# Performance work log

Measured on AMD Instinct MI355X. Metric: run time of the kernel, lower is better.

## Reference

```python
import jax, jax.numpy as jnp
import numpy as np

N_GRAPHS = 2048
BN_EPS = 1e-5


def _lin_init(k, fan_in, fan_out):
    kw, kb = jax.random.split(k)
    s = 1.0 / np.sqrt(fan_in)
    w = jax.random.uniform(kw, (fan_in, fan_out), minval=-s, maxval=s, dtype=jnp.float32)
    b = jax.random.uniform(kb, (fan_out,), minval=-s, maxval=s, dtype=jnp.float32)
    return w, b


def setup_inputs() -> dict:
    key = jax.random.key(0)
    ks = jax.random.split(key, 16)
    N, E, F, H, C = 100000, 600000, 7, 128, 2
    inp = {}
    inp["x"] = jax.random.normal(ks[0], (N, F), dtype=jnp.float32)
    inp["edge_index"] = jax.random.randint(ks[1], (2, E), 0, N)
    inp["edge_attr"] = jax.random.normal(ks[2], (E,), dtype=jnp.float32)  # ignored by GINConv
    inp["batch"] = jnp.sort(jax.random.randint(ks[3], (N,), 0, N_GRAPHS))
    # GINConv inner MLPs: [in, H, H]
    inp["g1_w1"], inp["g1_b1"] = _lin_init(ks[4], F, H)
    inp["g1_w2"], inp["g1_b2"] = _lin_init(ks[5], H, H)
    inp["g2_w1"], inp["g2_b1"] = _lin_init(ks[6], H, H)
    inp["g2_w2"], inp["g2_b2"] = _lin_init(ks[7], H, H)
    inp["g3_w1"], inp["g3_b1"] = _lin_init(ks[8], H, H)
    inp["g3_w2"], inp["g3_b2"] = _lin_init(ks[9], H, H)
    # JumpingKnowledge('cat') projection: 3H -> H
    inp["jk_w"], inp["jk_b"] = _lin_init(ks[10], 3 * H, H)
    # classifier MLP [H, H, C] with batch_norm on hidden layer
    inp["c1_w"], inp["c1_b"] = _lin_init(ks[11], H, H)
    inp["bn_g"] = jnp.ones((H,), jnp.float32)
    inp["bn_b"] = jnp.zeros((H,), jnp.float32)
    inp["c2_w"], inp["c2_b"] = _lin_init(ks[12], H, C)
    return inp


def reference(x, edge_index, edge_attr, batch,
              g1_w1, g1_b1, g1_w2, g1_b2,
              g2_w1, g2_b1, g2_w2, g2_b2,
              g3_w1, g3_b1, g3_w2, g3_b2,
              jk_w, jk_b, c1_w, c1_b, bn_g, bn_b, c2_w, c2_b):
    src, dst = edge_index[0], edge_index[1]
    N = x.shape[0]

    def gin_conv(h, w1, b1, w2, b2):
        # sum aggregation of neighbor messages; eps=0 -> (1+eps)*x + aggr = x + aggr
        agg = jax.ops.segment_sum(h[src], dst, num_segments=N)
        z = h + agg
        return jax.nn.relu(z @ w1 + b1) @ w2 + b2  # inner MLP, plain last layer

    # BasicGNN applies act (ReLU) after each conv; dropout=eval (identity)
    h1 = jax.nn.relu(gin_conv(x, g1_w1, g1_b1, g1_w2, g1_b2))
    h2 = jax.nn.relu(gin_conv(h1, g2_w1, g2_b1, g2_w2, g2_b2))
    h3 = jax.nn.relu(gin_conv(h2, g3_w1, g3_b1, g3_w2, g3_b2))

    h = jnp.concatenate([h1, h2, h3], axis=-1) @ jk_w + jk_b  # jk='cat' + final lin
    g = jax.ops.segment_sum(h, batch, num_segments=N_GRAPHS)  # global_add_pool -> [G, H]

    z = g @ c1_w + c1_b
    mu = z.mean(axis=0)
    var = z.var(axis=0)
    z = (z - mu) * jax.lax.rsqrt(var + BN_EPS) * bn_g + bn_b  # batch_norm (batch stats)
    z = jax.nn.relu(z)
    return z @ c2_w + c2_b  # [G, num_classes]
```

## Files before the change

### kernel.cpp

```cpp
#include <hip/hip_runtime.h>

#define NGRAPH 2048

typedef __attribute__((ext_vector_type(8))) short bf16x8;
typedef __attribute__((ext_vector_type(4))) float f32x4;
typedef __attribute__((ext_vector_type(8))) _Float16 h16x8;
typedef __attribute__((ext_vector_type(2))) _Float16 h16x2;

__device__ inline unsigned short bf16_rne(float f) {
  union { float f; unsigned u; } c; c.f = f;
  unsigned u = c.u + 0x7fffu + ((c.u >> 16) & 1u);
  return (unsigned short)(u >> 16);
}
__device__ inline float bf16_to_f32(unsigned short h) {
  union { float f; unsigned u; } c; c.u = ((unsigned)h) << 16;
  return c.f;
}

__global__ __launch_bounds__(256) void scan_onepass(
    const int* __restrict__ deg, int* __restrict__ rowstart, int* __restrict__ cursor,
    unsigned* __restrict__ scanst, int N, int E, int nchunk)
{
  __shared__ int tmp[256];
  __shared__ int sh_chunk;
  __shared__ int sh_exc;
  int tid = threadIdx.x;
  if (tid == 0) sh_chunk = (int)atomicAdd(&scanst[nchunk], 1u);
  __syncthreads();
  int cb = sh_chunk;
  int i = cb * 256 + tid;
  int v = (i < N) ? deg[i] : 0;
  tmp[tid] = v;
  __syncthreads();
#pragma unroll
  for (int off = 1; off < 256; off <<= 1) {
    int t = (tid >= off) ? tmp[tid - off] : 0;
    __syncthreads();
    tmp[tid] += t;
    __syncthreads();
  }
  int aggregate = tmp[255];

  if (tid == 0) {
    const unsigned VMASK = (1u << 30) - 1u;
    if (cb == 0) {
      atomicExch(&scanst[0], (2u << 30) | (unsigned)aggregate);
      sh_exc = 0;
    } else {
      atomicExch(&scanst[cb], (1u << 30) | (unsigned)aggregate);
      int excv = 0;
      int j = cb - 1;
      while (j >= 0) {
        unsigned s;
        do { s = atomicAdd(&scanst[j], 0u); } while ((s >> 30) == 0u);
        excv += (int)(s & VMASK);
        if ((s >> 30) == 2u) break;
        --j;
      }
      sh_exc = excv;
      atomicExch(&scanst[cb], (2u << 30) | (unsigned)(excv + aggregate));
    }
  }
  __syncthreads();
  int exc = sh_exc;
  if (i < N) {
    int rs = exc + tmp[tid] - v;
    rowstart[i] = rs;
    cursor[i] = rs;
  }
  if (cb == nchunk - 1 && tid == 0) rowstart[N] = E;
}

__global__ __launch_bounds__(256) void fill_eidx(
    const int* __restrict__ src, const int* __restrict__ dst,
    int* __restrict__ cursor, int* __restrict__ eidx, int E)
{
  int e = blockIdx.x * 256 + threadIdx.x;
  if (e >= E) return;
  int d = dst[e];
  int pos = atomicAdd(&cursor[d], 1);
  eidx[pos] = src[e];
}

struct WPs {
  const float* w[5];
  unsigned short* hi[5];
  unsigned short* lo[5];
};
__global__ __launch_bounds__(256) void prep_hist(
    WPs p, const float* __restrict__ x, _Float16* __restrict__ x8h, int N,
    const int* __restrict__ dst, int* __restrict__ deg, int E,
    const int* __restrict__ batch, int* __restrict__ gstart,
    float* __restrict__ bnstat)
{
  int g = blockIdx.x * 256 + threadIdx.x;
  if (g < E) {
    atomicAdd(&deg[dst[g]], 1);
    return;
  }
  int q = g - E;
  if (q < 5 * 16384) {
    int m = q >> 14;
    int j = q & 16383;
    int c = j >> 3, e = j & 7;
    int t = c >> 8, kc = (c >> 6) & 3, lane = c & 63;
    int n = t * 16 + (lane & 15);
    int k = kc * 32 + (lane >> 4) * 8 + e;
    float w = p.w[m][k * 128 + n];
    unsigned short h = bf16_rne(w);
    p.hi[m][j] = h;
    p.lo[m][j] = bf16_rne(w - bf16_to_f32(h));
    return;
  }
  q -= 5 * 16384;
  if (q < N * 8) {
    int v = q >> 3, j = q & 7;
    x8h[q] = (_Float16)((j < 7) ? x[(long)v * 7 + j] : 0.f);
    return;
  }
  q -= N * 8;
  if (q < 256) { bnstat[q] = 0.f; return; }
  q -= 256;
  if (q < N) {
    int b = batch[q];
    int bp = (q > 0) ? batch[q - 1] : -1;
    for (int gg = bp + 1; gg <= b; ++gg) gstart[gg] = q;
    if (q == N - 1)
      for (int gg = b + 1; gg <= NGRAPH; ++gg) gstart[gg] = N;
  }
}

__device__ inline void mfma_pass(
    const _Float16* __restrict__ zbuf,
    const unsigned short* __restrict__ Whi, const unsigned short* __restrict__ Wlo,
    int rw, int m16, int quad, int lane, f32x4 acc[8])
{
  int r = rw + m16;
  const _Float16* zrow = &zbuf[r * 128];
#pragma unroll
  for (int kc = 0; kc < 4; ++kc) {
    int cidx = kc * 4 + quad;
    h16x8 zh = *(const h16x8*)&zrow[((cidx + r) & 15) * 8];
    bf16x8 ah, al;
#pragma unroll
    for (int j = 0; j < 8; ++j) {
      float f = (float)zh[j];
      unsigned short h = bf16_rne(f);
      ah[j] = (short)h;
      al[j] = (short)bf16_rne(f - bf16_to_f32(h));
    }
#pragma unroll
    for (int t = 0; t < 8; ++t) {
      long cb = ((t * 4 + kc) * 64 + lane) * 8;
      bf16x8 bh = *(const bf16x8*)&Whi[cb];
      bf16x8 bl = *(const bf16x8*)&Wlo[cb];
      acc[t] = __builtin_amdgcn_mfma_f32_16x16x32_bf16(ah, bh, acc[t], 0, 0, 0);
      acc[t] = __builtin_amdgcn_mfma_f32_16x16x32_bf16(ah, bl, acc[t], 0, 0, 0);
      acc[t] = __builtin_amdgcn_mfma_f32_16x16x32_bf16(al, bh, acc[t], 0, 0, 0);
    }
  }
}

__global__ __launch_bounds__(256, 8) void fused_gin(
    const _Float16* __restrict__ H, const int* __restrict__ rowstart,
    const int* __restrict__ eidx,
    const unsigned short* __restrict__ W1hi, const unsigned short* __restrict__ W1lo,
    const float* __restrict__ B1,
    const unsigned short* __restrict__ W2hi, const unsigned short* __restrict__ W2lo,
    const float* __restrict__ B2,
    _Float16* __restrict__ Out, int M)
{
  __shared__ _Float16 zbuf[64 * 128];
  int tid = threadIdx.x;
  int rbase = blockIdx.x * 64;

  {
    int sub = tid & 15;
    int ng = tid >> 4;
    const _Float16* Hc = H + sub * 8;
#pragma unroll
    for (int it = 0; it < 4; ++it) {
      int r = it * 16 + ng;
      int v = rbase + r;
      int vc = (v < M) ? v : (M - 1);
      h16x8 sv = *(const h16x8*)&Hc[(long)vc * 128];
      float a0[8], a1[8];
#pragma unroll
      for (int j = 0; j < 8; ++j) { a0[j] = (float)sv[j]; a1[j] = 0.f; }
      int e0 = rowstart[vc], e1 = rowstart[vc + 1];
      int e = e0;
      for (; e + 4 <= e1; e += 4) {
        int s0 = eidx[e], s1 = eidx[e + 1], s2 = eidx[e + 2], s3 = eidx[e + 3];
        h16x8 h0 = *(const h16x8*)&Hc[(long)s0 * 128];
        h16x8 h1 = *(const h16x8*)&Hc[(long)s1 * 128];
        h16x8 h2 = *(const h16x8*)&Hc[(long)s2 * 128];
        h16x8 h3 = *(const h16x8*)&Hc[(long)s3 * 128];
#pragma unroll
        for (int j = 0; j < 8; ++j) {
          a0[j] += (float)h0[j] + (float)h2[j];
          a1[j] += (float)h1[j] + (float)h3[j];
        }
      }
      for (; e + 2 <= e1; e += 2) {
        int s0 = eidx[e], s1 = eidx[e + 1];
        h16x8 h0 = *(const h16x8*)&Hc[(long)s0 * 128];
        h16x8 h1 = *(const h16x8*)&Hc[(long)s1 * 128];
#pragma unroll
        for (int j = 0; j < 8; ++j) {
          a0[j] += (float)h0[j];
          a1[j] += (float)h1[j];
        }
      }
      if (e < e1) {
        int s = eidx[e];
        h16x8 h = *(const h16x8*)&Hc[(long)s * 128];
#pragma unroll
        for (int j = 0; j < 8; ++j) a1[j] += (float)h[j];
      }
      h16x8 zo;
#pragma unroll
      for (int j = 0; j < 8; ++j) zo[j] = (_Float16)(a0[j] + a1[j]);
      *(h16x8*)&zbuf[r * 128 + ((sub + r) & 15) * 8] = zo;
    }
  }
  __syncthreads();

  int lane = tid & 63;
  int wv = tid >> 6;
  int m16 = lane & 15;
  int quad = lane >> 4;
  int rw = wv * 16;

  f32x4 acc[8];
#pragma unroll
  for (int t = 0; t < 8; ++t) acc[t] = (f32x4){0.f, 0.f, 0.f, 0.f};
  mfma_pass(zbuf, W1hi, W1lo, rw, m16, quad, lane, acc);

  float bias[8];
#pragma unroll
  for (int t = 0; t < 8; ++t) bias[t] = B1[t * 16 + m16];

  __syncthreads();
#pragma unroll
  for (int i = 0; i < 4; ++i) {
    int r = rw + quad * 4 + i;
#pragma unroll
    for (int t = 0; t < 8; ++t) {
      int col = t * 16 + m16;
      int cidx = col >> 3;
      zbuf[r * 128 + ((cidx + r) & 15) * 8 + (col & 7)] =
          (_Float16)fmaxf(acc[t][i] + bias[t], 0.f);
    }
  }
  __syncthreads();

#pragma unroll
  for (int t = 0; t < 8; ++t) acc[t] = (f32x4){0.f, 0.f, 0.f, 0.f};
  mfma_pass(zbuf, W2hi, W2lo, rw, m16, quad, lane, acc);

#pragma unroll
  for (int t = 0; t < 8; ++t) bias[t] = B2[t * 16 + m16];

#pragma unroll
  for (int i = 0; i < 4; ++i) {
    int r = rbase + rw + quad * 4 + i;
    if (r < M) {
#pragma unroll
      for (int t = 0; t < 8; ++t) {
        float o = fmaxf(acc[t][i] + bias[t], 0.f);
        Out[(long)r * 128 + t * 16 + m16] = (_Float16)o;
      }
    }
  }
}

__global__ __launch_bounds__(256, 8) void fused_l1(
    const _Float16* __restrict__ x8h, const int* __restrict__ rowstart,
    const int* __restrict__ eidx,
    const float* __restrict__ W1, const float* __restrict__ B1,
    const unsigned short* __restrict__ W2hi, const unsigned short* __restrict__ W2lo,
    const float* __restrict__ B2, _Float16* __restrict__ Out, int M)
{
  __shared__ _Float16 ybuf[64 * 128];
  __shared__ float z1s[64][8];
  int tid = threadIdx.x;
  int rbase = blockIdx.x * 64;

  {
    int node = tid >> 2, sub = tid & 3;
    int v = rbase + node;
    int vc = (v < M) ? v : (M - 1);
    float a[8];
    if (sub == 0) {
      h16x8 sv = *(const h16x8*)&x8h[(long)vc * 8];
#pragma unroll
      for (int j = 0; j < 8; ++j) a[j] = (float)sv[j];
    } else {
#pragma unroll
      for (int j = 0; j < 8; ++j) a[j] = 0.f;
    }
    int e0 = rowstart[vc], e1 = rowstart[vc + 1];
    int e = e0 + sub;
    for (; e + 4 < e1; e += 8) {
      int s0 = eidx[e], s1 = eidx[e + 4];
      h16x8 h0 = *(const h16x8*)&x8h[(long)s0 * 8];
      h16x8 h1 = *(const h16x8*)&x8h[(long)s1 * 8];
#pragma unroll
      for (int j = 0; j < 8; ++j) a[j] += (float)h0[j] + (float)h1[j];
    }
    if (e < e1) {
      int s = eidx[e];
      h16x8 h = *(const h16x8*)&x8h[(long)s * 8];
#pragma unroll
      for (int j = 0; j < 8; ++j) a[j] += (float)h[j];
    }
#pragma unroll
    for (int j = 0; j < 8; ++j) {
      a[j] += __shfl_xor(a[j], 1, 64);
      a[j] += __shfl_xor(a[j], 2, 64);
    }
    if (sub == 0) {
#pragma unroll
      for (int j = 0; j < 8; ++j) z1s[node][j] = a[j];
    }
  }
  __syncthreads();

  {
    int c = tid & 127;
    int cidx = c >> 3, celt = c & 7;
    int rh0 = (tid >> 7) * 32;
    float w1r[7];
#pragma unroll
    for (int k = 0; k < 7; ++k) w1r[k] = W1[k * 128 + c];
    float b1 = B1[c];
#pragma unroll 4
    for (int rr = 0; rr < 32; ++rr) {
      int r = rh0 + rr;
      const float* zp = z1s[r];
      float a = b1;
#pragma unroll
      for (int k = 0; k < 7; ++k) a += zp[k] * w1r[k];
      ybuf[r * 128 + ((cidx + r) & 15) * 8 + celt] = (_Float16)fmaxf(a, 0.f);
    }
  }
  __syncthreads();

  int lane = tid & 63;
  int wv = tid >> 6;
  int m16 = lane & 15;
  int quad = lane >> 4;
  int rw = wv * 16;

  f32x4 acc[8];
#pragma unroll
  for (int t = 0; t < 8; ++t) acc[t] = (f32x4){0.f, 0.f, 0.f, 0.f};
  mfma_pass(ybuf, W2hi, W2lo, rw, m16, quad, lane, acc);

  float bias[8];
#pragma unroll
  for (int t = 0; t < 8; ++t) bias[t] = B2[t * 16 + m16];

#pragma unroll
  for (int i = 0; i < 4; ++i) {
    int r = rbase + rw + quad * 4 + i;
    if (r < M) {
#pragma unroll
      for (int t = 0; t < 8; ++t) {
        float o = fmaxf(acc[t][i] + bias[t], 0.f);
        Out[(long)r * 128 + t * 16 + m16] = (_Float16)o;
      }
    }
  }
}

__global__ __launch_bounds__(256) void pool_direct(
    const _Float16* __restrict__ H1, const _Float16* __restrict__ H2,
    const _Float16* __restrict__ H3, const int* __restrict__ gstart,
    float* __restrict__ P, float* __restrict__ cnt)
{
  int g = blockIdx.x;
  int s = gstart[g], e = gstart[g + 1];
  int tid = threadIdx.x;
  if (tid == 0) cnt[g] = (float)(e - s);
  if (tid >= 192) return;
  int cp = tid * 2;
  const _Float16* A = (cp < 128) ? H1 : ((cp < 256) ? H2 : H3);
  int c = cp & 127;
  float ax = 0.f, ay = 0.f, bx = 0.f, by = 0.f;
  int i = s;
  for (; i + 2 <= e; i += 2) {
    h16x2 v0 = *(const h16x2*)&A[(long)i * 128 + c];
    h16x2 v1 = *(const h16x2*)&A[(long)(i + 1) * 128 + c];
    ax += (float)v0[0]; ay += (float)v0[1];
    bx += (float)v1[0]; by += (float)v1[1];
  }
  if (i < e) {
    h16x2 v0 = *(const h16x2*)&A[(long)i * 128 + c];
    ax += (float)v0[0]; ay += (float)v0[1];
  }
  float2 o = {ax + bx, ay + by};
  *(float2*)&P[(long)g * 384 + cp] = o;
}

__global__ __launch_bounds__(256) void jk_gemm(
    const float* __restrict__ P, const float* __restrict__ cnt,
    const float* __restrict__ W, const float* __restrict__ B,
    float* __restrict__ G)
{
  __shared__ float pl[768];
  int tid = threadIdx.x, blk = blockIdx.x;
  for (int o = tid; o < 768; o += 256) pl[o] = P[(long)blk * 768 + o];
  __syncthreads();
  int rr = tid >> 7;
  int col = tid & 127;
  int row = blk * 2 + rr;
  float acc = cnt[row] * B[col];
#pragma unroll 8
  for (int k = 0; k < 384; ++k)
    acc += pl[rr * 384 + k] * W[k * 128 + col];
  G[(long)row * 128 + col] = acc;
}

__global__ __launch_bounds__(256) void gemm_bn(
    const float* __restrict__ Z,
    const float* __restrict__ W, const float* __restrict__ B,
    float* __restrict__ Out, float* __restrict__ bnstat, int M)
{
  __shared__ float wlds[128 * 128];
  int tid = threadIdx.x;
  {
    const float4* Ws = (const float4*)W;
    float4* Wd = (float4*)wlds;
#pragma unroll
    for (int i = 0; i < 16; ++i) Wd[i * 256 + tid] = Ws[i * 256 + tid];
  }
  __syncthreads();

  int rg = tid >> 5;
  int c0 = (tid & 31) * 4;
  int rbase = blockIdx.x * 64 + rg * 8;

  float acc[8][4];
#pragma unroll
  for (int i = 0; i < 8; ++i)
#pragma unroll
    for (int j = 0; j < 4; ++j) acc[i][j] = 0.f;

#pragma unroll 2
  for (int kc = 0; kc < 128; kc += 4) {
    float zv[8][4];
#pragma unroll
    for (int i = 0; i < 8; ++i) {
      float4 z = *(const float4*)&Z[(long)(rbase + i) * 128 + kc];
      zv[i][0] = z.x; zv[i][1] = z.y; zv[i][2] = z.z; zv[i][3] = z.w;
    }
#pragma unroll
    for (int kk = 0; kk < 4; ++kk) {
      float4 w = *(const float4*)&wlds[(kc + kk) * 128 + c0];
#pragma unroll
      for (int i = 0; i < 8; ++i) {
        float z = zv[i][kk];
        acc[i][0] += z * w.x; acc[i][1] += z * w.y;
        acc[i][2] += z * w.z; acc[i][3] += z * w.w;
      }
    }
  }

  float4 b = *(const float4*)&B[c0];
  float s[4] = {0.f, 0.f, 0.f, 0.f};
  float s2[4] = {0.f, 0.f, 0.f, 0.f};
#pragma unroll
  for (int i = 0; i < 8; ++i) {
    float4 o;
    o.x = acc[i][0] + b.x; o.y = acc[i][1] + b.y;
    o.z = acc[i][2] + b.z; o.w = acc[i][3] + b.w;
    *(float4*)&Out[(long)(rbase + i) * 128 + c0] = o;
    s[0] += o.x; s[1] += o.y; s[2] += o.z; s[3] += o.w;
    s2[0] += o.x * o.x; s2[1] += o.y * o.y; s2[2] += o.z * o.z; s2[3] += o.w * o.w;
  }
#pragma unroll
  for (int j = 0; j < 4; ++j) {
    atomicAdd(&bnstat[c0 + j], s[j]);
    atomicAdd(&bnstat[128 + c0 + j], s2[j]);
  }
}

__global__ __launch_bounds__(256) void bn_final(
    const float* __restrict__ ZC, const float* __restrict__ bnstat,
    const float* __restrict__ gma, const float* __restrict__ bta,
    const float* __restrict__ W2, const float* __restrict__ B2, float* __restrict__ out)
{
  __shared__ float scl[128], shf[128];
  int tid = threadIdx.x;
  if (tid < 128) {
    float mu = bnstat[tid] * (1.f / NGRAPH);
    float var = bnstat[128 + tid] * (1.f / NGRAPH) - mu * mu;
    float rs = rsqrtf(var + 1e-5f);
    float sc = gma[tid] * rs;
    scl[tid] = sc;
    shf[tid] = bta[tid] - mu * sc;
  }
  __syncthreads();
  int g = blockIdx.x * 256 + tid;
  if (g >= NGRAPH) return;
  float a0 = B2[0], a1 = B2[1];
#pragma unroll 4
  for (int h = 0; h < 128; ++h) {
    float zn = ZC[(long)g * 128 + h] * scl[h] + shf[h];
    zn = fmaxf(zn, 0.f);
    a0 += zn * W2[2 * h];
    a1 += zn * W2[2 * h + 1];
  }
  out[2 * g] = a0;
  out[2 * g + 1] = a1;
}

extern "C" void kernel_launch(void* const* d_in, const int* in_sizes, int n_in,
                              void* d_out, int out_size, void* d_ws, size_t ws_size,
                              hipStream_t stream)
{
  const float* x    = (const float*)d_in[0];
  const int*   ei   = (const int*)d_in[1];
  const int*   batch = (const int*)d_in[3];
  const float* g1w1 = (const float*)d_in[4];  const float* g1b1 = (const float*)d_in[5];
  const float* g1w2 = (const float*)d_in[6];  const float* g1b2 = (const float*)d_in[7];
  const float* g2w1 = (const float*)d_in[8];  const float* g2b1 = (const float*)d_in[9];
  const float* g2w2 = (const float*)d_in[10]; const float* g2b2 = (const float*)d_in[11];
  const float* g3w1 = (const float*)d_in[12]; const float* g3b1 = (const float*)d_in[13];
  const float* g3w2 = (const float*)d_in[14]; const float* g3b2 = (const float*)d_in[15];
  const float* jkw  = (const float*)d_in[16]; const float* jkb  = (const float*)d_in[17];
  const float* c1w  = (const float*)d_in[18]; const float* c1b  = (const float*)d_in[19];
  const float* bng  = (const float*)d_in[20]; const float* bnb  = (const float*)d_in[21];
  const float* c2w  = (const float*)d_in[22]; const float* c2b  = (const float*)d_in[23];

  const int N = in_sizes[3];
  const int E = in_sizes[1] / 2;
  const int* src = ei;
  const int* dst = ei + E;

  char* w = (char*)d_ws;
  auto alloc = [&](size_t bytes) {
    char* p = w;
    w += (bytes + 255) & ~(size_t)255;
    return p;
  };
  _Float16* hA = (_Float16*)alloc((size_t)N * 128 * 2);
  _Float16* hB = (_Float16*)alloc((size_t)N * 128 * 2);
  _Float16* hC = (_Float16*)alloc((size_t)N * 128 * 2);
  _Float16* x8h = (_Float16*)alloc((size_t)N * 8 * 2);
  float* P       = (float*)alloc((size_t)NGRAPH * 384 * 4);
  float* cnt     = (float*)alloc((size_t)NGRAPH * 4);
  float* bnstat  = (float*)alloc(256 * 4);
  float* gbuf = (float*)alloc((size_t)NGRAPH * 128 * 4);
  float* zc   = (float*)alloc((size_t)NGRAPH * 128 * 4);
  int* deg      = (int*)alloc((size_t)N * 4);
  unsigned* scanst = (unsigned*)alloc((size_t)1024 * 4);
  int* cursor   = (int*)alloc((size_t)N * 4);
  int* rowstart = (int*)alloc((size_t)(N + 1) * 4);
  int* eidx     = (int*)alloc((size_t)E * 4);
  int* gstart   = (int*)alloc((size_t)(NGRAPH + 1) * 4);
  unsigned short* wtbuf = (unsigned short*)alloc((size_t)5 * 2 * 16384 * 2);

  unsigned short* WThi[5];
  unsigned short* WTlo[5];
  for (int m = 0; m < 5; ++m) {
    WThi[m] = wtbuf + (size_t)m * 2 * 16384;
    WTlo[m] = WThi[m] + 16384;
  }

  const int nchunk = (N + 255) / 256;
  const int eb = (E + 255) / 256;

  hipMemsetAsync(deg, 0, (size_t)((char*)(scanst + 1024) - (char*)deg), stream);

  {
    WPs p;
    p.w[0] = g1w2; p.w[1] = g2w1; p.w[2] = g2w2; p.w[3] = g3w1; p.w[4] = g3w2;
    for (int m = 0; m < 5; ++m) { p.hi[m] = WThi[m]; p.lo[m] = WTlo[m]; }
    int total = E + 5 * 16384 + N * 8 + 256 + N;
    prep_hist<<<(total + 255) / 256, 256, 0, stream>>>(p, x, x8h, N, dst, deg, E,
                                                       batch, gstart, bnstat);
  }

  scan_onepass<<<nchunk, 256, 0, stream>>>(deg, rowstart, cursor, scanst, N, E, nchunk);
  fill_eidx<<<eb, 256, 0, stream>>>(src, dst, cursor, eidx, E);

  const int fBlocks = (N + 63) / 64;

  fused_l1<<<fBlocks, 256, 0, stream>>>(x8h, rowstart, eidx, g1w1, g1b1,
      WThi[0], WTlo[0], g1b2, hC, N);
  fused_gin<<<fBlocks, 256, 0, stream>>>(hC, rowstart, eidx,
      WThi[1], WTlo[1], g2b1, WThi[2], WTlo[2], g2b2, hB, N);
  fused_gin<<<fBlocks, 256, 0, stream>>>(hB, rowstart, eidx,
      WThi[3], WTlo[3], g3b1, WThi[4], WTlo[4], g3b2, hA, N);

  pool_direct<<<NGRAPH, 256, 0, stream>>>(hC, hB, hA, gstart, P, cnt);

  jk_gemm<<<NGRAPH / 2, 256, 0, stream>>>(P, cnt, jkw, jkb, gbuf);
  gemm_bn<<<NGRAPH / 64, 256, 0, stream>>>(gbuf, c1w, c1b, zc, bnstat, NGRAPH);
  bn_final<<<(NGRAPH + 255) / 256, 256, 0, stream>>>(zc, bnstat, bng, bnb, c2w, c2b, (float*)d_out);
}
```

Baseline: 410.4 us.

## Split fused GIN layer into separate gather kernel and MLP kernel

Layers 2 and 3 no longer aggregate neighbours inside the MFMA MLP kernel. A standalone gather kernel now sums neighbour features into a temporary fp16 buffer, and a new mlp2 kernel reads that buffer into LDS before running the two matmuls. The aim is to stop the irregular, latency-bound gather from stalling the MFMA work and to give each phase its own occupancy. In exchange it adds an extra N×128 fp16 write and read per layer plus two more kernel launches.

```diff
diff --git a/kernel.cpp b/kernel.cpp
--- a/kernel.cpp
+++ b/kernel.cpp
@@ -130,6 +130,55 @@
   }
 }
 
+__global__ __launch_bounds__(256) void gather_h(
+    const _Float16* __restrict__ H, const int* __restrict__ rowstart,
+    const int* __restrict__ eidx, _Float16* __restrict__ Z, int M)
+{
+  long t = (long)blockIdx.x * 256 + threadIdx.x;
+  int v = (int)(t >> 4);
+  if (v >= M) return;
+  int sub = (int)(t & 15);
+  const _Float16* Hc = H + sub * 8;
+  h16x8 sv = *(const h16x8*)&Hc[(long)v * 128];
+  float a0[8], a1[8];
+#pragma unroll
+  for (int j = 0; j < 8; ++j) { a0[j] = (float)sv[j]; a1[j] = 0.f; }
+  int e0 = rowstart[v], e1 = rowstart[v + 1];
+  int e = e0;
+  for (; e + 4 <= e1; e += 4) {
+    int s0 = eidx[e], s1 = eidx[e + 1], s2 = eidx[e + 2], s3 = eidx[e + 3];
+    h16x8 h0 = *(const h16x8*)&Hc[(long)s0 * 128];
+    h16x8 h1 = *(const h16x8*)&Hc[(long)s1 * 128];
+    h16x8 h2 = *(const h16x8*)&Hc[(long)s2 * 128];
+    h16x8 h3 = *(const h16x8*)&Hc[(long)s3 * 128];
+#pragma unroll
+    for (int j = 0; j < 8; ++j) {
+      a0[j] += (float)h0[j] + (float)h2[j];
+      a1[j] += (float)h1[j] + (float)h3[j];
+    }
+  }
+  for (; e + 2 <= e1; e += 2) {
+    int s0 = eidx[e], s1 = eidx[e + 1];
+    h16x8 h0 = *(const h16x8*)&Hc[(long)s0 * 128];
+    h16x8 h1 = *(const h16x8*)&Hc[(long)s1 * 128];
+#pragma unroll
+    for (int j = 0; j < 8; ++j) {
+      a0[j] += (float)h0[j];
+      a1[j] += (float)h1[j];
+    }
+  }
+  if (e < e1) {
+    int s = eidx[e];
+    h16x8 h = *(const h16x8*)&Hc[(long)s * 128];
+#pragma unroll
+    for (int j = 0; j < 8; ++j) a1[j] += (float)h[j];
+  }
+  h16x8 zo;
+#pragma unroll
+  for (int j = 0; j < 8; ++j) zo[j] = (_Float16)(a0[j] + a1[j]);
+  *(h16x8*)&Z[(long)v * 128 + sub * 8] = zo;
+}
+
 __device__ inline void mfma_pass(
     const _Float16* __restrict__ zbuf,
     const unsigned short* __restrict__ Whi, const unsigned short* __restrict__ Wlo,
@@ -161,9 +210,8 @@
   }
 }
 
-__global__ __launch_bounds__(256, 8) void fused_gin(
-    const _Float16* __restrict__ H, const int* __restrict__ rowstart,
-    const int* __restrict__ eidx,
+__global__ __launch_bounds__(256, 8) void mlp2(
+    const _Float16* __restrict__ Zin,
     const unsigned short* __restrict__ W1hi, const unsigned short* __restrict__ W1lo,
     const float* __restrict__ B1,
     const unsigned short* __restrict__ W2hi, const unsigned short* __restrict__ W2lo,
@@ -177,50 +225,13 @@
   {
     int sub = tid & 15;
     int ng = tid >> 4;
-    const _Float16* Hc = H + sub * 8;
 #pragma unroll
     for (int it = 0; it < 4; ++it) {
       int r = it * 16 + ng;
       int v = rbase + r;
       int vc = (v < M) ? v : (M - 1);
-      h16x8 sv = *(const h16x8*)&Hc[(long)vc * 128];
-      float a0[8], a1[8];
-#pragma unroll
-      for (int j = 0; j < 8; ++j) { a0[j] = (float)sv[j]; a1[j] = 0.f; }
-      int e0 = rowstart[vc], e1 = rowstart[vc + 1];
-      int e = e0;
-      for (; e + 4 <= e1; e += 4) {
-        int s0 = eidx[e], s1 = eidx[e + 1], s2 = eidx[e + 2], s3 = eidx[e + 3];
-        h16x8 h0 = *(const h16x8*)&Hc[(long)s0 * 128];
-        h16x8 h1 = *(const h16x8*)&Hc[(long)s1 * 128];
-        h16x8 h2 = *(const h16x8*)&Hc[(long)s2 * 128];
-        h16x8 h3 = *(const h16x8*)&Hc[(long)s3 * 128];
-#pragma unroll
-        for (int j = 0; j < 8; ++j) {
-          a0[j] += (float)h0[j] + (float)h2[j];
-          a1[j] += (float)h1[j] + (float)h3[j];
-        }
-      }
-      for (; e + 2 <= e1; e += 2) {
-        int s0 = eidx[e], s1 = eidx[e + 1];
-        h16x8 h0 = *(const h16x8*)&Hc[(long)s0 * 128];
-        h16x8 h1 = *(const h16x8*)&Hc[(long)s1 * 128];
-#pragma unroll
-        for (int j = 0; j < 8; ++j) {
-          a0[j] += (float)h0[j];
-          a1[j] += (float)h1[j];
-        }
-      }
-      if (e < e1) {
-        int s = eidx[e];
-        h16x8 h = *(const h16x8*)&Hc[(long)s * 128];
-#pragma unroll
-        for (int j = 0; j < 8; ++j) a1[j] += (float)h[j];
-      }
-      h16x8 zo;
-#pragma unroll
-      for (int j = 0; j < 8; ++j) zo[j] = (_Float16)(a0[j] + a1[j]);
-      *(h16x8*)&zbuf[r * 128 + ((sub + r) & 15) * 8] = zo;
+      h16x8 zi = *(const h16x8*)&Zin[(long)vc * 128 + sub * 8];
+      *(h16x8*)&zbuf[r * 128 + ((sub + r) & 15) * 8] = zi;
     }
   }
   __syncthreads();
@@ -548,6 +559,7 @@
   _Float16* hA = (_Float16*)alloc((size_t)N * 128 * 2);
   _Float16* hB = (_Float16*)alloc((size_t)N * 128 * 2);
   _Float16* hC = (_Float16*)alloc((size_t)N * 128 * 2);
+  _Float16* zt = (_Float16*)alloc((size_t)N * 128 * 2);
   _Float16* x8h = (_Float16*)alloc((size_t)N * 8 * 2);
   float* P       = (float*)alloc((size_t)NGRAPH * 384 * 4);
   float* cnt     = (float*)alloc((size_t)NGRAPH * 4);
@@ -587,13 +599,18 @@
   fill_eidx<<<eb, 256, 0, stream>>>(src, dst, cursor, eidx, E);
 
   const int fBlocks = (N + 63) / 64;
+  const int gBlocks = (int)(((long)N * 16 + 255) / 256);
 
   fused_l1<<<fBlocks, 256, 0, stream>>>(x8h, rowstart, eidx, g1w1, g1b1,
       WThi[0], WTlo[0], g1b2, hC, N);
-  fused_gin<<<fBlocks, 256, 0, stream>>>(hC, rowstart, eidx,
-      WThi[1], WTlo[1], g2b1, WThi[2], WTlo[2], g2b2, hB, N);
-  fused_gin<<<fBlocks, 256, 0, stream>>>(hB, rowstart, eidx,
-      WThi[3], WTlo[3], g3b1, WThi[4], WTlo[4], g3b2, hA, N);
+
+  gather_h<<<gBlocks, 256, 0, stream>>>(hC, rowstart, eidx, zt, N);
+  mlp2<<<fBlocks, 256, 0, stream>>>(zt, WThi[1], WTlo[1], g2b1,
+      WThi[2], WTlo[2], g2b2, hB, N);
+
+  gather_h<<<gBlocks, 256, 0, stream>>>(hB, rowstart, eidx, zt, N);
+  mlp2<<<fBlocks, 256, 0, stream>>>(zt, WThi[3], WTlo[3], g3b1,
+      WThi[4], WTlo[4], g3b2, hA, N);
 
   pool_direct<<<NGRAPH, 256, 0, stream>>>(hC, hB, hA, gstart, P, cnt);
 
```

Result: slower. 435.9 us (+6.2%).
